# Kernel optimization log

Hardware: AMD Instinct MI355X
Metric: run time of the kernel (lower is better)

The kernel has to match this reference:

```python
import jax, jax.numpy as jnp
import numpy as np

B, N, D, H, K, T = 32, 4096, 256, 4, 8, 3
D_H = D // H
SCALE = D_H ** -0.5
EPS = 1e-8
LN_EPS = 1e-5


def _ln(x, g, b):
    m = x.mean(-1, keepdims=True)
    v = ((x - m) ** 2).mean(-1, keepdims=True)
    return (x - m) / jnp.sqrt(v + LN_EPS) * g + b


def _split(t):  # [b, n, D] -> [b, H, n, d_h]
    b, n, _ = t.shape
    return t.reshape(b, n, H, D_H).transpose(0, 2, 1, 3)


def _merge(t):  # [b, H, n, d_h] -> [b, n, D]
    b, h, n, d = t.shape
    return t.transpose(0, 2, 1, 3).reshape(b, n, h * d)


def setup_inputs() -> dict:
    key = jax.random.key(0)
    ks = jax.random.split(key, 12)
    init = lambda k, shape: (jax.random.normal(k, shape, jnp.float32) * 0.02)
    mu = jnp.tile(jnp.linspace(-1.0, 1.0, K)[:, None], (1, D))[None]  # [1,K,D]
    return {
        'x': jax.random.normal(ks[0], (B, N, D), jnp.float32),
        'mu': mu,
        'w_q': init(ks[1], (D, D)),
        'w_k': init(ks[2], (D, D)),
        'w_v': init(ks[3], (D, D)),
        'w_comb': init(ks[4], (D, D)),
        'g_in': jnp.ones(D), 'b_in': jnp.zeros(D),
        'g_slot': jnp.ones(D), 'b_slot': jnp.zeros(D),
        'g_mlp': jnp.ones(D), 'b_mlp': jnp.zeros(D),
        'w_ih': init(ks[5], (3 * D, D)),
        'w_hh': init(ks[6], (3 * D, D)),
        'b_ih': jnp.zeros(3 * D),
        'b_hh': jnp.zeros(3 * D),
        'w1': init(ks[7], (D, D)), 'b1': jnp.zeros(D),
        'w2': init(ks[8], (D, D)), 'b2': jnp.zeros(D),
    }


def reference(x, mu, w_q, w_k, w_v, w_comb, g_in, b_in, g_slot, b_slot,
              g_mlp, b_mlp, w_ih, w_hh, b_ih, b_hh, w1, b1, w2, b2):
    b = x.shape[0]
    x_norm = _ln(x, g_in, b_in)
    k_feat = _split(x_norm @ w_k.T)  # [b,H,N,d_h]
    v_feat = _split(x_norm @ w_v.T)

    def gru(u, h):  # torch GRUCell semantics
        gi = u @ w_ih.T + b_ih
        gh = h @ w_hh.T + b_hh
        ir, iz, i_n = jnp.split(gi, 3, axis=-1)
        hr, hz, h_n = jnp.split(gh, 3, axis=-1)
        r = jax.nn.sigmoid(ir + hr)
        z = jax.nn.sigmoid(iz + hz)
        n = jnp.tanh(i_n + r * h_n)
        return (1.0 - z) * n + z * h

    def step(slots, _):
        q = _split(_ln(slots, g_slot, b_slot) @ w_q.T)  # [b,H,K,d_h]
        dots = jnp.einsum('bhkd,bhnd->bhkn', q, k_feat) * SCALE
        attn = jax.nn.softmax(dots, axis=-2)  # softmax over slots
        attn = attn / (attn.sum(axis=-1, keepdims=True) + EPS)  # renorm over inputs
        updates = _merge(jnp.einsum('bhkn,bhnd->bhkd', attn, v_feat)) @ w_comb.T
        new = gru(updates.reshape(-1, D), slots.reshape(-1, D)).reshape(slots.shape)
        hid = jnp.maximum(_ln(new, g_mlp, b_mlp) @ w1.T + b1, 0.0)
        new = new + (hid @ w2.T + b2)
        return new, None

    slots0 = jnp.broadcast_to(mu, (b, K, D))  # eval mode: slots = mu
    slots, _ = jax.lax.scan(step, slots0, None, length=T)
    return slots
```

## Files before the change

kernel.cpp:

```cpp
#include <hip/hip_runtime.h>

#define BB 32
#define NN 4096
#define DD 256
#define HH 4
#define KK 8
#define DH 64

typedef unsigned short u16;
typedef unsigned int u32;
typedef __attribute__((ext_vector_type(8))) short short8;
typedef __attribute__((ext_vector_type(4))) float f32x4;

__device__ __forceinline__ float b2f(u16 u){ return __uint_as_float(((u32)u)<<16); }
__device__ __forceinline__ u16 f2b(float f){
  u32 u = __float_as_uint(f);
  u32 r = (u + 0x7fffu + ((u>>16)&1u)) >> 16;
  return (u16)r;
}

__global__ __launch_bounds__(256) void prep_kernel(
    const float* __restrict__ mu, const float* __restrict__ w_q,
    const float* __restrict__ w_k, const float* __restrict__ w_v,
    const float* __restrict__ w_comb, const float* __restrict__ w_ih,
    const float* __restrict__ w_hh, const float* __restrict__ w1,
    const float* __restrict__ w2,
    u16* __restrict__ wkv, u16* __restrict__ wq_b, u16* __restrict__ wcomb_b,
    u16* __restrict__ wih_b, u16* __restrict__ whh_b, u16* __restrict__ w1_b,
    u16* __restrict__ w2_b, float* __restrict__ slots)
{
  int i = blockIdx.x*256 + threadIdx.x;
  if (i < 131072) {
    wkv[i] = f2b((i < 65536) ? w_k[i] : w_v[i-65536]);
    return;
  }
  i -= 131072;
  if (i < 65536){ wq_b[i] = f2b(w_q[i]); return; } i -= 65536;
  if (i < 65536){ wcomb_b[i] = f2b(w_comb[i]); return; } i -= 65536;
  if (i < 196608){ wih_b[i] = f2b(w_ih[i]); return; } i -= 196608;
  if (i < 196608){ whh_b[i] = f2b(w_hh[i]); return; } i -= 196608;
  if (i < 65536){ w1_b[i] = f2b(w1[i]); return; } i -= 65536;
  if (i < 65536){ w2_b[i] = f2b(w2[i]); return; } i -= 65536;
  if (i < 65536){ slots[i] = mu[i & 2047]; return; }
}

__global__ __launch_bounds__(512,4) void kv_proj_kernel(
    const float* __restrict__ x, const float* __restrict__ g_in,
    const float* __restrict__ b_in, const u16* __restrict__ wkv,
    u16* __restrict__ Kmat, u16* __restrict__ Vmat)
{
  __shared__ __align__(16) u16 Atile[64*256];
  __shared__ __align__(16) u16 Cbuf[2][64*64];
  const int tid = threadIdx.x;
  const int w = tid>>6, l = tid&63;
  const long row0 = (long)blockIdx.x * 64;
  const int wm = w>>2, wn = w&3;
  const int lr = l&15, lk = (l>>4)*8;

  const u16* bp = wkv + (wn*16 + lr)*256 + lk;
  short8 bf[8];
  #pragma unroll
  for (int ks=0;ks<8;++ks) bf[ks] = *(const short8*)(bp + ks*32);

  f32x4 xr[8];
  #pragma unroll
  for (int rr=0;rr<8;++rr)
    xr[rr] = *(const f32x4*)(x + (row0 + w*8 + rr)*DD + l*4);

  const f32x4 gv = *(const f32x4*)(g_in + l*4);
  const f32x4 bv = *(const f32x4*)(b_in + l*4);

  #pragma unroll
  for (int rr=0; rr<8; ++rr) {
    const int r = w*8 + rr;
    const f32x4 xv = xr[rr];
    float s = xv.x+xv.y+xv.z+xv.w;
    float s2 = xv.x*xv.x+xv.y*xv.y+xv.z*xv.z+xv.w*xv.w;
    #pragma unroll
    for (int m=1;m<64;m<<=1){ s += __shfl_xor(s,m); s2 += __shfl_xor(s2,m); }
    const float mean = s * (1.f/256.f);
    const float rstd = rsqrtf(s2*(1.f/256.f) - mean*mean + 1e-5f);
    const u32 p0 = (u32)f2b((xv.x-mean)*rstd*gv.x + bv.x) | ((u32)f2b((xv.y-mean)*rstd*gv.y + bv.y)<<16);
    const u32 p1 = (u32)f2b((xv.z-mean)*rstd*gv.z + bv.z) | ((u32)f2b((xv.w-mean)*rstd*gv.w + bv.w)<<16);
    const unsigned long long pp = (unsigned long long)p0 | ((unsigned long long)p1<<32);
    *(unsigned long long*)((char*)Atile + r*512 + ((l*8) ^ ((r&15)<<4))) = pp;
  }
  __syncthreads();

  short8 afr0[8], afr1[8];
  #pragma unroll
  for (int ks=0;ks<8;++ks) {
    const int k2 = (ks*32 + lk)*2;
    { const int r = wm*32 + lr;      afr0[ks] = *(const short8*)((const char*)Atile + r*512 + (k2 ^ ((r&15)<<4))); }
    { const int r = wm*32 + 16 + lr; afr1[ks] = *(const short8*)((const char*)Atile + r*512 + (k2 ^ ((r&15)<<4))); }
  }

  #pragma unroll
  for (int ct=0; ct<8; ++ct) {
    if (ct > 0) {
      const int r = tid>>3, cg = tid&7;
      const short8 vv = *(const short8*)((char*)Cbuf[(ct-1)&1] + r*128 + ((cg*16) ^ ((r&7)<<4)));
      u16* dst = ((ct-1)<4) ? Kmat : Vmat;
      *(short8*)(dst + (row0+r)*DD + ((ct-1)&3)*64 + cg*8) = vv;
    }

    f32x4 acc0 = (f32x4)0.f, acc1 = (f32x4)0.f;
    #pragma unroll
    for (int ks=0;ks<8;++ks) {
      acc0 = __builtin_amdgcn_mfma_f32_16x16x32_bf16(afr0[ks], bf[ks], acc0, 0,0,0);
      acc1 = __builtin_amdgcn_mfma_f32_16x16x32_bf16(afr1[ks], bf[ks], acc1, 0,0,0);
    }

    if (ct < 7) {
      #pragma unroll
      for (int ks=0;ks<8;++ks) bf[ks] = *(const short8*)(bp + (ct+1)*16384 + ks*32);
    }

    {
      const int c = wn*16 + lr;
      #pragma unroll
      for (int reg=0; reg<4; ++reg) {
        const int r0r = wm*32 + (l>>4)*4 + reg;
        const int r1r = r0r + 16;
        *(u16*)((char*)Cbuf[ct&1] + r0r*128 + ((2*c) ^ ((r0r&7)<<4))) = f2b(acc0[reg]);
        *(u16*)((char*)Cbuf[ct&1] + r1r*128 + ((2*c) ^ ((r1r&7)<<4))) = f2b(acc1[reg]);
      }
    }
    __syncthreads();
  }
  {
    const int r = tid>>3, cg = tid&7;
    const short8 vv = *(const short8*)((char*)Cbuf[1] + r*128 + ((cg*16) ^ ((r&7)<<4)));
    *(short8*)(Vmat + (row0+r)*DD + 3*64 + cg*8) = vv;
  }
}

__global__ __launch_bounds__(256) void slot_q_kernel(
    const float* __restrict__ slots, const float* __restrict__ g_slot,
    const float* __restrict__ b_slot, const u16* __restrict__ wq_b,
    float* __restrict__ qmat)
{
  __shared__ float xn[256];
  __shared__ float red[8];
  const int r = blockIdx.x, t = threadIdx.x;
  const int w = t>>6, l = t&63;
  const float xv = slots[r*256 + t];
  float s = xv, s2 = xv*xv;
  #pragma unroll
  for (int m=1;m<64;m<<=1){ s += __shfl_xor(s,m); s2 += __shfl_xor(s2,m); }
  if (l==0){ red[w*2]=s; red[w*2+1]=s2; }
  __syncthreads();
  s = red[0]+red[2]+red[4]+red[6];
  s2 = red[1]+red[3]+red[5]+red[7];
  const float mean = s*(1.f/256.f);
  const float rstd = rsqrtf(s2*(1.f/256.f)-mean*mean + 1e-5f);
  xn[t] = (xv-mean)*rstd*g_slot[t] + b_slot[t];
  __syncthreads();
  const u16* wr = wq_b + t*256;
  float a0=0,a1=0,a2=0,a3=0;
  for (int d=0; d<256; d+=8) {
    const short8 wv = *(const short8*)(wr + d);
    a0 = fmaf(b2f((u16)wv[0]), xn[d+0], a0);
    a1 = fmaf(b2f((u16)wv[1]), xn[d+1], a1);
    a2 = fmaf(b2f((u16)wv[2]), xn[d+2], a2);
    a3 = fmaf(b2f((u16)wv[3]), xn[d+3], a3);
    a0 = fmaf(b2f((u16)wv[4]), xn[d+4], a0);
    a1 = fmaf(b2f((u16)wv[5]), xn[d+5], a1);
    a2 = fmaf(b2f((u16)wv[6]), xn[d+6], a2);
    a3 = fmaf(b2f((u16)wv[7]), xn[d+7], a3);
  }
  qmat[r*256 + t] = ((a0+a1)+(a2+a3));
}

__global__ __launch_bounds__(256) void attn_kernel(
    const u16* __restrict__ Kmat, const u16* __restrict__ Vmat,
    const float* __restrict__ qmat, float* __restrict__ U_part,
    float* __restrict__ S_part)
{
  __shared__ float U_lds[4][8][64];
  __shared__ float S_lds[4][8];
  const int bid = blockIdx.x;
  const int part = bid & 3, h = (bid>>2)&3, b = bid>>4;
  const int t = threadIdx.x, w = t>>6, l = t&63;
  const int ds = l&7, ng = l>>3;

  float qreg[8][8];
  #pragma unroll
  for (int k=0;k<8;++k) {
    const f32x4 qa = *(const f32x4*)(qmat + (b*8+k)*256 + h*64 + ds*8);
    const f32x4 qb = *(const f32x4*)(qmat + (b*8+k)*256 + h*64 + ds*8 + 4);
    qreg[k][0]=qa.x; qreg[k][1]=qa.y; qreg[k][2]=qa.z; qreg[k][3]=qa.w;
    qreg[k][4]=qb.x; qreg[k][5]=qb.y; qreg[k][6]=qb.z; qreg[k][7]=qb.w;
  }

  float accU[8][8];
  float sacc[8];
  #pragma unroll
  for (int k=0;k<8;++k){ sacc[k]=0.f;
    #pragma unroll
    for (int j=0;j<8;++j) accU[k][j]=0.f; }

  const long base = ((long)b*NN)*DD + h*64;
  const u16* Kp = Kmat + base + (long)(part*1024 + w*8 + ng)*DD + ds*8;
  const u16* Vp = Vmat + base + (long)(part*1024 + w*8 + ng)*DD + ds*8;

  short8 kc = *(const short8*)Kp;
  short8 vc = *(const short8*)Vp;
  for (int pass=0; pass<32; ++pass) {
    short8 kn, vn;
    if (pass < 31) {
      kn = *(const short8*)(Kp + (pass+1)*32*DD);
      vn = *(const short8*)(Vp + (pass+1)*32*DD);
    }
    float kd[8];
    #pragma unroll
    for (int j=0;j<8;++j) kd[j] = b2f((u16)kc[j]);
    float dots[8];
    #pragma unroll
    for (int k=0;k<8;++k) {
      float d0 = qreg[k][0]*kd[0] + qreg[k][1]*kd[1] + qreg[k][2]*kd[2] + qreg[k][3]*kd[3]
               + qreg[k][4]*kd[4] + qreg[k][5]*kd[5] + qreg[k][6]*kd[6] + qreg[k][7]*kd[7];
      d0 += __shfl_xor(d0,1); d0 += __shfl_xor(d0,2); d0 += __shfl_xor(d0,4);
      dots[k] = d0 * 0.125f;
    }
    float mx = dots[0];
    #pragma unroll
    for (int k=1;k<8;++k) mx = fmaxf(mx, dots[k]);
    float e[8]; float se = 0.f;
    #pragma unroll
    for (int k=0;k<8;++k){ e[k] = __expf(dots[k]-mx); se += e[k]; }
    const float inv = 1.f/se;
    float vd[8];
    #pragma unroll
    for (int j=0;j<8;++j) vd[j] = b2f((u16)vc[j]);
    #pragma unroll
    for (int k=0;k<8;++k) {
      const float p = e[k]*inv;
      sacc[k] += p;
      #pragma unroll
      for (int j=0;j<8;++j) accU[k][j] = fmaf(p, vd[j], accU[k][j]);
    }
    kc = kn; vc = vn;
  }
  #pragma unroll
  for (int k=0;k<8;++k){
    #pragma unroll
    for (int j=0;j<8;++j){
      float v = accU[k][j];
      v += __shfl_xor(v,8); v += __shfl_xor(v,16); v += __shfl_xor(v,32);
      accU[k][j]=v;
    }
    float sv = sacc[k];
    sv += __shfl_xor(sv,8); sv += __shfl_xor(sv,16); sv += __shfl_xor(sv,32);
    sacc[k]=sv;
  }
  if (l<8){
    #pragma unroll
    for (int k=0;k<8;++k)
      #pragma unroll
      for (int j=0;j<8;++j) U_lds[w][k][l*8+j] = accU[k][j];
  }
  if (l==0){
    #pragma unroll
    for (int k=0;k<8;++k) S_lds[w][k]=sacc[k];
  }
  __syncthreads();
  for (int i=t;i<512;i+=256){
    const int k=i>>6, d=i&63;
    U_part[(((long)part*32 + b)*4 + h)*512 + k*64 + d] =
      U_lds[0][k][d]+U_lds[1][k][d]+U_lds[2][k][d]+U_lds[3][k][d];
  }
  if (t<8){
    S_part[((part*32 + b)*4 + h)*8 + t] = S_lds[0][t]+S_lds[1][t]+S_lds[2][t]+S_lds[3][t];
  }
}

__global__ __launch_bounds__(256) void slot_update_kernel(
    const float* __restrict__ U_part, const float* __restrict__ S_part,
    float* __restrict__ slots,
    const u16* __restrict__ wcomb_b, const u16* __restrict__ wih_b,
    const u16* __restrict__ whh_b, const u16* __restrict__ w1_b,
    const u16* __restrict__ w2_b,
    const float* __restrict__ b_ih, const float* __restrict__ b_hh,
    const float* __restrict__ g_mlp, const float* __restrict__ b_mlp,
    const float* __restrict__ b1v, const float* __restrict__ b2v,
    const u16* __restrict__ wq_b, const float* __restrict__ g_slot,
    const float* __restrict__ b_slot, float* __restrict__ qmat,
    float* __restrict__ out_final, const int write_out, const int compute_q)
{
  __shared__ float uL[2][256];
  __shared__ float hL[2][256];
  __shared__ float cL[2][256];
  __shared__ float xL[2][256];
  __shared__ float red[16];
  const int blk = blockIdx.x, t = threadIdx.x;
  const int w = t>>6, l = t&63;
  const int r0 = blk*2;

  #pragma unroll
  for (int rr=0;rr<2;++rr) hL[rr][t] = slots[(r0+rr)*256 + t];

  #pragma unroll
  for (int rr=0;rr<2;++rr) {
    const int r = r0+rr, b = r>>3, k = r&7;
    const int h = t>>6, d = t&63;
    float ssum = 0.f, usum = 0.f;
    #pragma unroll
    for (int p=0;p<4;++p) {
      ssum += S_part[((p*32 + b)*4 + h)*8 + k];
      usum += U_part[(((long)p*32 + b)*4 + h)*512 + k*64 + d];
    }
    uL[rr][t] = usum / (ssum + 1e-8f);
  }
  __syncthreads();

  {
    float c00=0,c01=0,c10=0,c11=0;
    const u16* wr = wcomb_b + t*256;
    for (int d0=0; d0<256; d0+=8) {
      const short8 wv = *(const short8*)(wr + d0);
      float wf[8];
      #pragma unroll
      for (int j=0;j<8;++j) wf[j]=b2f((u16)wv[j]);
      #pragma unroll
      for (int j=0;j<8;j+=2) {
        c00 = fmaf(wf[j],   uL[0][d0+j],   c00);
        c01 = fmaf(wf[j+1], uL[0][d0+j+1], c01);
        c10 = fmaf(wf[j],   uL[1][d0+j],   c10);
        c11 = fmaf(wf[j+1], uL[1][d0+j+1], c11);
      }
    }
    cL[0][t]=c00+c01; cL[1][t]=c10+c11;
  }
  __syncthreads();

  float gi[3][2], gh[3][2];
  #pragma unroll
  for (int g=0; g<3; ++g){ gi[g][0]=0; gi[g][1]=0; gh[g][0]=0; gh[g][1]=0; }
  for (int d0=0; d0<256; d0+=8) {
    float u0[8],u1[8],h0[8],h1[8];
    #pragma unroll
    for (int j=0;j<8;j+=4) {
      *(f32x4*)&u0[j] = *(const f32x4*)&cL[0][d0+j];
      *(f32x4*)&u1[j] = *(const f32x4*)&cL[1][d0+j];
      *(f32x4*)&h0[j] = *(const f32x4*)&hL[0][d0+j];
      *(f32x4*)&h1[j] = *(const f32x4*)&hL[1][d0+j];
    }
    #pragma unroll
    for (int g=0; g<3; ++g) {
      const short8 wi = *(const short8*)(wih_b + (g*256+t)*256 + d0);
      const short8 wh = *(const short8*)(whh_b + (g*256+t)*256 + d0);
      #pragma unroll
      for (int j=0;j<8;++j) {
        const float a = b2f((u16)wi[j]);
        const float bw = b2f((u16)wh[j]);
        gi[g][0] = fmaf(a, u0[j], gi[g][0]);
        gi[g][1] = fmaf(a, u1[j], gi[g][1]);
        gh[g][0] = fmaf(bw, h0[j], gh[g][0]);
        gh[g][1] = fmaf(bw, h1[j], gh[g][1]);
      }
    }
  }
  float newv[2];
  #pragma unroll
  for (int rr=0;rr<2;++rr) {
    const float ir = gi[0][rr] + b_ih[t];
    const float iz = gi[1][rr] + b_ih[256+t];
    const float inn= gi[2][rr] + b_ih[512+t];
    const float hr = gh[0][rr] + b_hh[t];
    const float hz = gh[1][rr] + b_hh[256+t];
    const float hn = gh[2][rr] + b_hh[512+t];
    const float rg = 1.f/(1.f + __expf(-(ir+hr)));
    const float zg = 1.f/(1.f + __expf(-(iz+hz)));
    float targ = inn + rg*hn;
    targ = fminf(fmaxf(targ, -15.f), 15.f);
    const float ex = __expf(2.f*targ);
    const float ng = (ex-1.f)/(ex+1.f);
    newv[rr] = (1.f-zg)*ng + zg*hL[rr][t];
  }

  float s0=newv[0], q0=newv[0]*newv[0], s1=newv[1], q1=newv[1]*newv[1];
  #pragma unroll
  for (int m=1;m<64;m<<=1){
    s0+=__shfl_xor(s0,m); q0+=__shfl_xor(q0,m);
    s1+=__shfl_xor(s1,m); q1+=__shfl_xor(q1,m);
  }
  if (l==0){ red[w*4]=s0; red[w*4+1]=q0; red[w*4+2]=s1; red[w*4+3]=q1; }
  __syncthreads();
  s0 = red[0]+red[4]+red[8]+red[12];
  q0 = red[1]+red[5]+red[9]+red[13];
  s1 = red[2]+red[6]+red[10]+red[14];
  q1 = red[3]+red[7]+red[11]+red[15];
  {
    const float m0 = s0*(1.f/256.f), m1 = s1*(1.f/256.f);
    const float r0v = rsqrtf(q0*(1.f/256.f)-m0*m0 + 1e-5f);
    const float r1v = rsqrtf(q1*(1.f/256.f)-m1*m1 + 1e-5f);
    xL[0][t] = (newv[0]-m0)*r0v*g_mlp[t] + b_mlp[t];
    xL[1][t] = (newv[1]-m1)*r1v*g_mlp[t] + b_mlp[t];
  }
  __syncthreads();

  {
    float c00=0,c01=0,c10=0,c11=0;
    const u16* wr = w1_b + t*256;
    for (int d0=0; d0<256; d0+=8) {
      const short8 wv = *(const short8*)(wr + d0);
      float wf[8];
      #pragma unroll
      for (int j=0;j<8;++j) wf[j]=b2f((u16)wv[j]);
      #pragma unroll
      for (int j=0;j<8;j+=2) {
        c00 = fmaf(wf[j],   xL[0][d0+j],   c00);
        c01 = fmaf(wf[j+1], xL[0][d0+j+1], c01);
        c10 = fmaf(wf[j],   xL[1][d0+j],   c10);
        c11 = fmaf(wf[j+1], xL[1][d0+j+1], c11);
      }
    }
    uL[0][t] = fmaxf(c00+c01 + b1v[t], 0.f);
    uL[1][t] = fmaxf(c10+c11 + b1v[t], 0.f);
  }
  __syncthreads();

  float o0, o1;
  {
    float c00=0,c01=0,c10=0,c11=0;
    const u16* wr = w2_b + t*256;
    for (int d0=0; d0<256; d0+=8) {
      const short8 wv = *(const short8*)(wr + d0);
      float wf[8];
      #pragma unroll
      for (int j=0;j<8;++j) wf[j]=b2f((u16)wv[j]);
      #pragma unroll
      for (int j=0;j<8;j+=2) {
        c00 = fmaf(wf[j],   uL[0][d0+j],   c00);
        c01 = fmaf(wf[j+1], uL[0][d0+j+1], c01);
        c10 = fmaf(wf[j],   uL[1][d0+j],   c10);
        c11 = fmaf(wf[j+1], uL[1][d0+j+1], c11);
      }
    }
    o0 = newv[0] + c00+c01 + b2v[t];
    o1 = newv[1] + c10+c11 + b2v[t];
    slots[(r0+0)*256 + t] = o0;
    slots[(r0+1)*256 + t] = o1;
    if (write_out){
      out_final[(r0+0)*256 + t] = o0;
      out_final[(r0+1)*256 + t] = o1;
    }
  }

  if (compute_q) {
    __syncthreads();
    float t0=o0, p0=o0*o0, t1=o1, p1=o1*o1;
    #pragma unroll
    for (int m=1;m<64;m<<=1){
      t0+=__shfl_xor(t0,m); p0+=__shfl_xor(p0,m);
      t1+=__shfl_xor(t1,m); p1+=__shfl_xor(p1,m);
    }
    if (l==0){ red[w*4]=t0; red[w*4+1]=p0; red[w*4+2]=t1; red[w*4+3]=p1; }
    __syncthreads();
    t0 = red[0]+red[4]+red[8]+red[12];
    p0 = red[1]+red[5]+red[9]+red[13];
    t1 = red[2]+red[6]+red[10]+red[14];
    p1 = red[3]+red[7]+red[11]+red[15];
    const float m0 = t0*(1.f/256.f), m1 = t1*(1.f/256.f);
    const float r0v = rsqrtf(p0*(1.f/256.f)-m0*m0 + 1e-5f);
    const float r1v = rsqrtf(p1*(1.f/256.f)-m1*m1 + 1e-5f);
    cL[0][t] = (o0-m0)*r0v*g_slot[t] + b_slot[t];
    cL[1][t] = (o1-m1)*r1v*g_slot[t] + b_slot[t];
    __syncthreads();
    float c00=0,c01=0,c10=0,c11=0;
    const u16* wr = wq_b + t*256;
    for (int d0=0; d0<256; d0+=8) {
      const short8 wv = *(const short8*)(wr + d0);
      float wf[8];
      #pragma unroll
      for (int j=0;j<8;++j) wf[j]=b2f((u16)wv[j]);
      #pragma unroll
      for (int j=0;j<8;j+=2) {
        c00 = fmaf(wf[j],   cL[0][d0+j],   c00);
        c01 = fmaf(wf[j+1], cL[0][d0+j+1], c01);
        c10 = fmaf(wf[j],   cL[1][d0+j],   c10);
        c11 = fmaf(wf[j+1], cL[1][d0+j+1], c11);
      }
    }
    qmat[(r0+0)*256 + t] = c00+c01;
    qmat[(r0+1)*256 + t] = c10+c11;
  }
}

extern "C" void kernel_launch(void* const* d_in, const int* in_sizes, int n_in,
                              void* d_out, int out_size, void* d_ws, size_t ws_size,
                              hipStream_t stream)
{
  (void)in_sizes; (void)n_in; (void)out_size; (void)ws_size;
  const float* x      = (const float*)d_in[0];
  const float* mu     = (const float*)d_in[1];
  const float* w_q    = (const float*)d_in[2];
  const float* w_k    = (const float*)d_in[3];
  const float* w_v    = (const float*)d_in[4];
  const float* w_comb = (const float*)d_in[5];
  const float* g_in   = (const float*)d_in[6];
  const float* b_in   = (const float*)d_in[7];
  const float* g_slot = (const float*)d_in[8];
  const float* b_slot = (const float*)d_in[9];
  const float* g_mlp  = (const float*)d_in[10];
  const float* b_mlp  = (const float*)d_in[11];
  const float* w_ih   = (const float*)d_in[12];
  const float* w_hh   = (const float*)d_in[13];
  const float* b_ih   = (const float*)d_in[14];
  const float* b_hh   = (const float*)d_in[15];
  const float* w1     = (const float*)d_in[16];
  const float* b1     = (const float*)d_in[17];
  const float* w2     = (const float*)d_in[18];
  const float* b2     = (const float*)d_in[19];

  char* ws = (char*)d_ws;
  u16* Kmat    = (u16*)(ws + 0);
  u16* Vmat    = (u16*)(ws + 67108864);
  u16* wkv     = (u16*)(ws + 134217728);
  u16* wq_b    = (u16*)(ws + 134479872);
  u16* wcomb_b = (u16*)(ws + 134610944);
  u16* wih_b   = (u16*)(ws + 134742016);
  u16* whh_b   = (u16*)(ws + 135135232);
  u16* w1_b    = (u16*)(ws + 135528448);
  u16* w2_b    = (u16*)(ws + 135659520);
  float* slots = (float*)(ws + 135790592);
  float* qmat  = (float*)(ws + 136052736);
  float* U_part= (float*)(ws + 136314880);
  float* S_part= (float*)(ws + 137363456);

  hipLaunchKernelGGL(prep_kernel, dim3(3328), dim3(256), 0, stream,
                     mu, w_q, w_k, w_v, w_comb, w_ih, w_hh, w1, w2,
                     wkv, wq_b, wcomb_b, wih_b, whh_b, w1_b, w2_b, slots);
  hipLaunchKernelGGL(kv_proj_kernel, dim3(2048), dim3(512), 0, stream,
                     x, g_in, b_in, wkv, Kmat, Vmat);
  hipLaunchKernelGGL(slot_q_kernel, dim3(256), dim3(256), 0, stream,
                     slots, g_slot, b_slot, wq_b, qmat);
  float* outp = (float*)d_out;
  for (int it=0; it<3; ++it) {
    hipLaunchKernelGGL(attn_kernel, dim3(512), dim3(256), 0, stream,
                       Kmat, Vmat, qmat, U_part, S_part);
    hipLaunchKernelGGL(slot_update_kernel, dim3(128), dim3(256), 0, stream,
                       U_part, S_part, slots, wcomb_b, wih_b, whh_b, w1_b, w2_b,
                       b_ih, b_hh, g_mlp, b_mlp, b1, b2,
                       wq_b, g_slot, b_slot, qmat,
                       outp, (it==2)?1:0, (it<2)?1:0);
  }
}
```

Measured before the change: 412.3 us.

## Stage K/V weight tiles in swizzled LDS via coalesced loads in kv_proj

The prep kernel now writes the combined K/V weight in an XOR-swizzled row layout so that kv_proj can fetch each 64-column weight chunk with fully coalesced 16-byte loads and copy it straight into an LDS tile. Each wave then reads its B fragments from LDS instead of issuing strided per-lane global loads. The C buffer is no longer double-buffered, so the loop gains a second barrier per column tile, and the x rows are loaded inside the LayerNorm loop rather than prefetched. The change is meant to cut redundant global weight traffic and improve load coalescing, at the cost of 32 KB more LDS, which may lower occupancy, plus the extra synchronisation.

```diff
diff --git a/kernel.cpp b/kernel.cpp
--- a/kernel.cpp
+++ b/kernel.cpp
@@ -31,7 +31,10 @@
 {
   int i = blockIdx.x*256 + threadIdx.x;
   if (i < 131072) {
-    wkv[i] = f2b((i < 65536) ? w_k[i] : w_v[i-65536]);
+    int c = i>>8, d = i&255;
+    float v = (c<256) ? w_k[c*256+d] : w_v[(c-256)*256+d];
+    int off = (c<<9) + ((2*d) ^ ((c&15)<<4));
+    wkv[off>>1] = f2b(v);
     return;
   }
   i -= 131072;
@@ -50,22 +53,16 @@
     u16* __restrict__ Kmat, u16* __restrict__ Vmat)
 {
   __shared__ __align__(16) u16 Atile[64*256];
-  __shared__ __align__(16) u16 Cbuf[2][64*64];
+  __shared__ __align__(16) u16 Btile[64*256];
+  __shared__ __align__(16) u16 Cbuf[64*64];
   const int tid = threadIdx.x;
   const int w = tid>>6, l = tid&63;
   const long row0 = (long)blockIdx.x * 64;
-  const int wm = w>>2, wn = w&3;
-  const int lr = l&15, lk = (l>>4)*8;
-
-  const u16* bp = wkv + (wn*16 + lr)*256 + lk;
-  short8 bf[8];
-  #pragma unroll
-  for (int ks=0;ks<8;++ks) bf[ks] = *(const short8*)(bp + ks*32);
-
-  f32x4 xr[8];
-  #pragma unroll
-  for (int rr=0;rr<8;++rr)
-    xr[rr] = *(const f32x4*)(x + (row0 + w*8 + rr)*DD + l*4);
+
+  short8 breg[4];
+  #pragma unroll
+  for (int i=0;i<4;++i)
+    breg[i] = *(const short8*)((const char*)wkv + (i*512 + tid)*16);
 
   const f32x4 gv = *(const f32x4*)(g_in + l*4);
   const f32x4 bv = *(const f32x4*)(b_in + l*4);
@@ -73,7 +70,7 @@
   #pragma unroll
   for (int rr=0; rr<8; ++rr) {
     const int r = w*8 + rr;
-    const f32x4 xv = xr[rr];
+    const f32x4 xv = *(const f32x4*)(x + (row0+r)*DD + l*4);
     float s = xv.x+xv.y+xv.z+xv.w;
     float s2 = xv.x*xv.x+xv.y*xv.y+xv.z*xv.z+xv.w*xv.w;
     #pragma unroll
@@ -85,35 +82,46 @@
     const unsigned long long pp = (unsigned long long)p0 | ((unsigned long long)p1<<32);
     *(unsigned long long*)((char*)Atile + r*512 + ((l*8) ^ ((r&15)<<4))) = pp;
   }
-  __syncthreads();
+  #pragma unroll
+  for (int i=0;i<4;++i)
+    *(short8*)((char*)Btile + (i*512+tid)*16) = breg[i];
+  __syncthreads();
+
+  const int wm = w>>2, wn = w&3;
+  const int lr = l&15;
+  const int lk = (l>>4)*8;
 
   short8 afr0[8], afr1[8];
   #pragma unroll
-  for (int ks=0;ks<8;++ks) {
+  for (int ks=0; ks<8; ++ks) {
     const int k2 = (ks*32 + lk)*2;
-    { const int r = wm*32 + lr;      afr0[ks] = *(const short8*)((const char*)Atile + r*512 + (k2 ^ ((r&15)<<4))); }
-    { const int r = wm*32 + 16 + lr; afr1[ks] = *(const short8*)((const char*)Atile + r*512 + (k2 ^ ((r&15)<<4))); }
-  }
-
-  #pragma unroll
+    const int r0r = wm*32 + lr;
+    const int r1r = wm*32 + 16 + lr;
+    afr0[ks] = *(const short8*)((const char*)Atile + r0r*512 + (k2 ^ ((r0r&15)<<4)));
+    afr1[ks] = *(const short8*)((const char*)Atile + r1r*512 + (k2 ^ ((r1r&15)<<4)));
+  }
+  #pragma unroll
+  for (int ks=0; ks<8; ++ks) {
+    asm volatile("" : "+v"(afr0[ks]));
+    asm volatile("" : "+v"(afr1[ks]));
+  }
+
   for (int ct=0; ct<8; ++ct) {
-    if (ct > 0) {
-      const int r = tid>>3, cg = tid&7;
-      const short8 vv = *(const short8*)((char*)Cbuf[(ct-1)&1] + r*128 + ((cg*16) ^ ((r&7)<<4)));
-      u16* dst = ((ct-1)<4) ? Kmat : Vmat;
-      *(short8*)(dst + (row0+r)*DD + ((ct-1)&3)*64 + cg*8) = vv;
+    short8 nreg[4];
+    if (ct < 7) {
+      #pragma unroll
+      for (int i=0;i<4;++i)
+        nreg[i] = *(const short8*)((const char*)wkv + (ct+1)*32768 + (i*512 + tid)*16);
     }
 
     f32x4 acc0 = (f32x4)0.f, acc1 = (f32x4)0.f;
     #pragma unroll
-    for (int ks=0;ks<8;++ks) {
-      acc0 = __builtin_amdgcn_mfma_f32_16x16x32_bf16(afr0[ks], bf[ks], acc0, 0,0,0);
-      acc1 = __builtin_amdgcn_mfma_f32_16x16x32_bf16(afr1[ks], bf[ks], acc1, 0,0,0);
-    }
-
-    if (ct < 7) {
-      #pragma unroll
-      for (int ks=0;ks<8;++ks) bf[ks] = *(const short8*)(bp + (ct+1)*16384 + ks*32);
+    for (int ks=0; ks<8; ++ks) {
+      const int k2 = (ks*32 + lk)*2;
+      const int c = wn*16 + lr;
+      const short8 bfv = *(const short8*)((const char*)Btile + c*512 + (k2 ^ ((c&15)<<4)));
+      acc0 = __builtin_amdgcn_mfma_f32_16x16x32_bf16(afr0[ks], bfv, acc0, 0,0,0);
+      acc1 = __builtin_amdgcn_mfma_f32_16x16x32_bf16(afr1[ks], bfv, acc1, 0,0,0);
     }
 
     {
@@ -122,16 +130,24 @@
       for (int reg=0; reg<4; ++reg) {
         const int r0r = wm*32 + (l>>4)*4 + reg;
         const int r1r = r0r + 16;
-        *(u16*)((char*)Cbuf[ct&1] + r0r*128 + ((2*c) ^ ((r0r&7)<<4))) = f2b(acc0[reg]);
-        *(u16*)((char*)Cbuf[ct&1] + r1r*128 + ((2*c) ^ ((r1r&7)<<4))) = f2b(acc1[reg]);
+        *(u16*)((char*)Cbuf + r0r*128 + ((2*c) ^ ((r0r&7)<<4))) = f2b(acc0[reg]);
+        *(u16*)((char*)Cbuf + r1r*128 + ((2*c) ^ ((r1r&7)<<4))) = f2b(acc1[reg]);
       }
     }
     __syncthreads();
-  }
-  {
-    const int r = tid>>3, cg = tid&7;
-    const short8 vv = *(const short8*)((char*)Cbuf[1] + r*128 + ((cg*16) ^ ((r&7)<<4)));
-    *(short8*)(Vmat + (row0+r)*DD + 3*64 + cg*8) = vv;
+
+    if (ct < 7) {
+      #pragma unroll
+      for (int i=0;i<4;++i)
+        *(short8*)((char*)Btile + (i*512+tid)*16) = nreg[i];
+    }
+    {
+      const int r = tid>>3, cg = tid&7;
+      const short8 vv = *(const short8*)((char*)Cbuf + r*128 + ((cg*16) ^ ((r&7)<<4)));
+      u16* dst = (ct<4) ? Kmat : Vmat;
+      *(short8*)(dst + (row0+r)*DD + (ct&3)*64 + cg*8) = vv;
+    }
+    __syncthreads();
   }
 }
 
```

New measurement: 350.2 us. 1.18x faster.
